# Optimization experiments

Measured on AMD Instinct MI355X. Metric: run time of the kernel, lower is better.

Reference implementation:

```python
import jax, jax.numpy as jnp
import numpy as np

EPS = 1e-3  # keras LayerNormalization default epsilon

def _layernorm(x, g, b):
    mu = jnp.mean(x, axis=-1, keepdims=True)
    var = jnp.mean(jnp.square(x - mu), axis=-1, keepdims=True)
    return (x - mu) * jax.lax.rsqrt(var + EPS) * g + b

def setup_inputs() -> dict:
    key = jax.random.key(0)
    ks = jax.random.split(key, 12)
    B, T, C = 2, 2048, 768
    s = 0.02
    return {
        "x": jax.random.normal(ks[0], (B, T, C), jnp.float32),
        "ln1_g": jnp.ones((C,), jnp.float32), "ln1_b": jnp.zeros((C,), jnp.float32),
        "Wq": jax.random.normal(ks[1], (C, C), jnp.float32) * s, "bq": jnp.zeros((C,), jnp.float32),
        "Wk": jax.random.normal(ks[2], (C, C), jnp.float32) * s, "bk": jnp.zeros((C,), jnp.float32),
        "Wv": jax.random.normal(ks[3], (C, C), jnp.float32) * s, "bv": jnp.zeros((C,), jnp.float32),
        "ln2_g": jnp.ones((C,), jnp.float32), "ln2_b": jnp.zeros((C,), jnp.float32),
        "W1": jax.random.normal(ks[4], (C, 4 * C), jnp.float32) * s, "b1": jnp.zeros((4 * C,), jnp.float32),
        "W2": jax.random.normal(ks[5], (4 * C, C), jnp.float32) * s, "b2": jnp.zeros((C,), jnp.float32),
    }

def reference(x, ln1_g, ln1_b, Wq, bq, Wk, bk, Wv, bv, ln2_g, ln2_b, W1, b1, W2, b2):
    H = 12
    B, T, C = x.shape
    dh = C // H
    # pre-LN (note: original overwrites x with LN output before residual)
    x = _layernorm(x, ln1_g, ln1_b)
    q = (x @ Wq + bq).reshape(B, T, H, dh).transpose(0, 2, 1, 3)
    k = (x @ Wk + bk).reshape(B, T, H, dh).transpose(0, 2, 1, 3)
    v = (x @ Wv + bv).reshape(B, T, H, dh).transpose(0, 2, 1, 3)
    # original computes K @ Q^T (transpose_b on query)
    scores = jnp.einsum('bhid,bhjd->bhij', k, q) / jnp.sqrt(jnp.float32(dh))
    mask = jnp.tril(jnp.ones((T, T), bool))
    scores = jnp.where(mask, scores, -jnp.inf)
    p = jax.nn.softmax(scores, axis=-1)
    y = jnp.einsum('bhij,bhjd->bhid', p, v)  # [B,H,T,dh]
    y = y.transpose(0, 2, 1, 3).reshape(B, T, C)
    x = x + y
    h = _layernorm(x, ln2_g, ln2_b)
    h = jax.nn.gelu(h @ W1 + b1, approximate=False)
    h = h @ W2 + b2
    return x + h
```

## Files before the change

kernel.cpp:

```cpp
#include <hip/hip_runtime.h>
#include <hip/hip_bf16.h>
#include <cmath>


#define BB 2
#define TT 2048
#define CC 768
#define HH 12
#define DH 64
#define NROWS (BB*TT)
#define NHEADS (BB*HH)

typedef __attribute__((ext_vector_type(8))) short bf16x8;
typedef __attribute__((ext_vector_type(4))) float f32x4;
typedef __attribute__((ext_vector_type(4))) unsigned short u16x4;

__device__ __forceinline__ unsigned short f2bf(float f){
  union { __hip_bfloat16 h; unsigned short u; } c;
  c.h = __float2bfloat16(f);
  return c.u;
}
__device__ __forceinline__ float bf2f(unsigned short u){
  union { unsigned int i; float f; } x; x.i = ((unsigned int)u) << 16; return x.f;
}
template<int BK>
__device__ __forceinline__ int swzk(int r, int c){
  if constexpr (BK == 64) return (r << 6) + (c ^ ((r & 7) << 3));
  else                    return (r << 5) + (c ^ (((r >> 1) & 3) << 3));
}
template<int BK>
__device__ __forceinline__ int swzsrc(int r, int c){
  if constexpr (BK == 64) return c ^ ((r & 7) << 3);
  else                    return c ^ (((r >> 1) & 3) << 3);
}
__device__ __forceinline__ float wred_sum(float v){
  #pragma unroll
  for(int m = 1; m < 64; m <<= 1) v += __shfl_xor(v, m, 64);
  return v;
}
__device__ __forceinline__ float gelu_fast(float x){
  float x2 = x * x;
  float e = x * fmaf(x2, 0.044715f, 1.0f) * 2.30203136f;
  float t = exp2f(e);
  return x - x / (t + 1.0f);
}
__device__ __forceinline__ void gload_lds16(const void* g, void* l){
  __builtin_amdgcn_global_load_lds((const __attribute__((address_space(1))) void*)g,
                                   (__attribute__((address_space(3))) void*)l, 16, 0, 0);
}
template<int N> __device__ __forceinline__ void waitcnt_vm(){
  if constexpr (N == 0)      asm volatile("s_waitcnt vmcnt(0)" ::: "memory");
  else if constexpr (N == 4) asm volatile("s_waitcnt vmcnt(4)" ::: "memory");
  else if constexpr (N == 8) asm volatile("s_waitcnt vmcnt(8)" ::: "memory");
  else static_assert(N == 0 || N == 4 || N == 8, "unsupported vmcnt");
}

#define SCLOG2 (0.125f * 1.44269504f)

__device__ __forceinline__ void tc_body(const float* __restrict__ in,
                                        unsigned short* __restrict__ out,
                                        int K, int N, int bx, int by,
                                        float (*tile)[33]){
  int n0 = bx * 32, k0 = by * 32;
  int t = threadIdx.x; int c = t & 31; int r0 = t >> 5;
  #pragma unroll
  for(int p = 0; p < 4; p++){
    int r = r0 + p * 8;
    tile[r][c] = in[(size_t)(k0 + r) * N + n0 + c];
  }
  __syncthreads();
  #pragma unroll
  for(int p = 0; p < 4; p++){
    int r = r0 + p * 8;
    out[(size_t)(n0 + r) * K + k0 + c] = f2bf(tile[c][r]);
  }
}

__device__ __forceinline__ void ln_body(const float* __restrict__ in,
                                        const float* __restrict__ gm,
                                        const float* __restrict__ bt,
                                        unsigned short* __restrict__ out_b,
                                        int r){
  int t = threadIdx.x;
  const float* row = in + (size_t)r * CC;
  float v0 = row[t], v1 = row[t + 256], v2 = row[t + 512];
  float s = wred_sum(v0 + v1 + v2);
  __shared__ float red[4];
  if((t & 63) == 0) red[t >> 6] = s;
  __syncthreads();
  float mu = (red[0] + red[1] + red[2] + red[3]) * (1.0f / CC);
  float d0 = v0 - mu, d1 = v1 - mu, d2 = v2 - mu;
  float q = wred_sum(d0 * d0 + d1 * d1 + d2 * d2);
  __shared__ float red2[4];
  if((t & 63) == 0) red2[t >> 6] = q;
  __syncthreads();
  float var = (red2[0] + red2[1] + red2[2] + red2[3]) * (1.0f / CC);
  float rinv = rsqrtf(var + 1e-3f);
  float o0 = d0 * rinv * gm[t]       + bt[t];
  float o1 = d1 * rinv * gm[t + 256] + bt[t + 256];
  float o2 = d2 * rinv * gm[t + 512] + bt[t + 512];
  size_t base = (size_t)r * CC;
  out_b[base + t] = f2bf(o0); out_b[base + t + 256] = f2bf(o1); out_b[base + t + 512] = f2bf(o2);
}

__global__ __launch_bounds__(256) void prep_ln_kernel(const float* __restrict__ Wq,
                                                      const float* __restrict__ Wk,
                                                      const float* __restrict__ Wv,
                                                      const float* __restrict__ W1,
                                                      const float* __restrict__ W2,
                                                      const float* __restrict__ bq,
                                                      const float* __restrict__ bk,
                                                      const float* __restrict__ bv,
                                                      const float* __restrict__ x,
                                                      const float* __restrict__ ln1g,
                                                      const float* __restrict__ ln1b,
                                                      unsigned short* __restrict__ wqkv,
                                                      unsigned short* __restrict__ w1t,
                                                      unsigned short* __restrict__ w2t,
                                                      float* __restrict__ bqkv,
                                                      unsigned short* __restrict__ xlnb){
  __shared__ float tile[32][33];
  int o = blockIdx.x;
  if(o < 1728){
    int z = o / 576, r = o % 576;
    const float* in = (z == 0) ? Wq : (z == 1) ? Wk : Wv;
    tc_body(in, wqkv + (size_t)z * CC * CC, CC, CC, r % 24, r / 24, tile);
  } else if(o < 4032){
    int r = o - 1728;
    tc_body(W1, w1t, CC, 4 * CC, r % 96, r / 96, tile);
  } else if(o < 6336){
    int r = o - 4032;
    tc_body(W2, w2t, 4 * CC, CC, r % 24, r / 24, tile);
  } else if(o < 6345){
    int i = (o - 6336) * 256 + threadIdx.x;
    if(i < 3 * CC) bqkv[i] = (i < CC) ? bq[i] : (i < 2 * CC) ? bk[i - CC] : bv[i - 2 * CC];
  } else {
    ln_body(x, ln1g, ln1b, xlnb, o - 6345);
  }
}

template<int MODE, int TILE, int BK>
__global__ __launch_bounds__(256) void gemm_bt(const unsigned short* __restrict__ A,
                                               const unsigned short* __restrict__ Bt,
                                               const float* __restrict__ bias,
                                               const float* __restrict__ resid,
                                               void* __restrict__ outp,
                                               unsigned short* __restrict__ vt,
                                               int M, int N, int K){
  constexpr int F = TILE / 32;
  constexpr int SEGS = TILE * BK / 512;
  constexpr int R = SEGS / 4;
  constexpr int NLD = 2 * R;
  constexpr int LPR = BK / 8;
  constexpr int RPS = 512 / BK;
  __shared__ unsigned short As[3][TILE * BK];
  __shared__ unsigned short Bs[3][TILE * BK];
  int m0 = blockIdx.y * TILE, n0 = blockIdx.x * TILE;
  int t = threadIdx.x; int w = t >> 6; int l = t & 63;
  int g = l >> 4; int lc = l & 15;
  int wm = w >> 1, wn = w & 1;
  f32x4 zero4 = {0.f, 0.f, 0.f, 0.f};
  f32x4 acc[F][F];
  #pragma unroll
  for(int mi = 0; mi < F; mi++)
    #pragma unroll
    for(int ni = 0; ni < F; ni++) acc[mi][ni] = zero4;

  auto stage = [&](int ks, int cb){
    #pragma unroll
    for(int p = 0; p < R; p++){
      int sgi = w * R + p;
      int r = sgi * RPS + l / LPR;
      int c = (l % LPR) * 8;
      int csrc = swzsrc<BK>(r, c);
      gload_lds16(A  + (size_t)(m0 + r) * K + ks + csrc, &As[cb][sgi * 512]);
      gload_lds16(Bt + (size_t)(n0 + r) * K + ks + csrc, &Bs[cb][sgi * 512]);
    }
  };

  int nt = K / BK;
  stage(0, 0);
  if(nt > 1) stage(BK, 1);
  if(nt > 2) stage(2 * BK, 2);
  int cur = 0;
  for(int ti = 0; ti < nt; ti++){
    if(ti + 2 < nt)      waitcnt_vm<2 * NLD>();
    else if(ti + 1 < nt) waitcnt_vm<NLD>();
    else                 waitcnt_vm<0>();
    __builtin_amdgcn_s_barrier();
    #pragma unroll
    for(int kk = 0; kk < BK / 32; kk++){
      bf16x8 af[F], bfv[F];
      #pragma unroll
      for(int mi = 0; mi < F; mi++) af[mi]  = *(const bf16x8*)&As[cur][swzk<BK>(wm * (TILE / 2) + mi * 16 + lc, kk * 32 + g * 8)];
      #pragma unroll
      for(int ni = 0; ni < F; ni++) bfv[ni] = *(const bf16x8*)&Bs[cur][swzk<BK>(wn * (TILE / 2) + ni * 16 + lc, kk * 32 + g * 8)];
      #pragma unroll
      for(int mi = 0; mi < F; mi++)
        #pragma unroll
        for(int ni = 0; ni < F; ni++)
          acc[mi][ni] = __builtin_amdgcn_mfma_f32_16x16x32_bf16(af[mi], bfv[ni], acc[mi][ni], 0, 0, 0);
    }
    __builtin_amdgcn_s_barrier();
    if(ti + 3 < nt) stage((ti + 3) * BK, cur);
    cur = (cur == 2) ? 0 : cur + 1;
  }
  #pragma unroll
  for(int mi = 0; mi < F; mi++)
    #pragma unroll
    for(int ni = 0; ni < F; ni++){
      int col = n0 + wn * (TILE / 2) + ni * 16 + lc;
      float bvv = bias[col];
      if(MODE == 3 && col >= 2 * CC){
        int hh = (col - 2 * CC) >> 6, d = (col - 2 * CC) & 63;
        int rowb = m0 + wm * (TILE / 2) + mi * 16 + g * 4;
        int bb = rowb >> 11, tb = rowb & 2047;
        u16x4 pk;
        #pragma unroll
        for(int rr = 0; rr < 4; rr++) pk[rr] = f2bf(acc[mi][ni][rr] + bvv);
        *(u16x4*)&vt[(((size_t)bb * HH + hh) * DH + d) * TT + tb] = pk;
      } else {
        #pragma unroll
        for(int rr = 0; rr < 4; rr++){
          int row = m0 + wm * (TILE / 2) + mi * 16 + g * 4 + rr;
          float v = acc[mi][ni][rr] + bvv;
          size_t idx = (size_t)row * N + col;
          if(MODE == 1) v = gelu_fast(v);
          if(MODE == 2) ((float*)outp)[idx] = v + resid[idx];
          else          ((unsigned short*)outp)[idx] = f2bf(v);
        }
      }
    }
}

__global__ __launch_bounds__(256) void attn_kernel(const unsigned short* __restrict__ qkv,
                                                   const unsigned short* __restrict__ vt,
                                                   unsigned short* __restrict__ po,
                                                   float* __restrict__ pl,
                                                   float* __restrict__ pm){
  __shared__ unsigned short Aq[2][64 * 64];
  __shared__ unsigned short Vs[2][64 * 64];
  __shared__ unsigned short Ps[4][16 * 64];
  int o = blockIdx.x;
  int xcd = o & 7, qq = o >> 3;
  int head = xcd * 3 + (qq % 3);
  int r_ = qq / 3;
  int bx = 31 - (r_ >> 1);
  int sp = r_ & 1;
  int b = head / HH, h = head % HH;
  int t = threadIdx.x; int w = t >> 6; int l = t & 63;
  int g = l >> 4, lc = l & 15;
  int i0w = bx * 64 + w * 16;
  int irow = i0w + lc;
  unsigned short* pw = &Ps[w][0];

  int hh = (bx + 2) >> 1;
  int js0 = sp ? hh : 0;
  int js1 = sp ? (bx + 1) : hh;

  int rl = l >> 3;
  int csrc = ((l & 7) * 8) ^ (rl * 8);

  bf16x8 bk[2];
  #pragma unroll
  for(int kk = 0; kk < 2; kk++)
    bk[kk] = *(const bf16x8*)(qkv + (size_t)(b * TT + irow) * (3 * CC) + CC + h * DH + kk * 32 + g * 8);

  float m_ = 0.0f, lsum = 0.f;
  f32x4 zero4 = {0.f, 0.f, 0.f, 0.f};
  f32x4 o4[4];
  #pragma unroll
  for(int ds = 0; ds < 4; ds++) o4[ds] = zero4;

  auto stage = [&](int j0, int cb){
    #pragma unroll
    for(int p = 0; p < 2; p++){
      int sgi = w * 2 + p;
      int row = sgi * 8 + rl;
      gload_lds16(qkv + (size_t)(b * TT + j0 + row) * (3 * CC) + h * DH + csrc, &Aq[cb][sgi * 512]);
      gload_lds16(vt  + (size_t)(head * DH + row) * TT + j0 + csrc,             &Vs[cb][sgi * 512]);
    }
  };

  if(js0 < js1){
    stage(js0 * 64, js0 & 1);
    if(js0 + 1 < js1) stage((js0 + 1) * 64, (js0 + 1) & 1);

    for(int jt = js0; jt < js1; jt++){
      int j0 = jt * 64;
      int buf = jt & 1;
      if(jt + 1 < js1) waitcnt_vm<4>(); else waitcnt_vm<0>();
      __builtin_amdgcn_s_barrier();
      f32x4 s[4];
      __builtin_amdgcn_s_setprio(1);
      #pragma unroll
      for(int js = 0; js < 4; js++){
        s[js] = zero4;
        #pragma unroll
        for(int kk = 0; kk < 2; kk++){
          bf16x8 aq = *(const bf16x8*)&Aq[buf][swzk<64>(js * 16 + lc, kk * 32 + g * 8)];
          s[js] = __builtin_amdgcn_mfma_f32_16x16x32_bf16(aq, bk[kk], s[js], 0, 0, 0);
        }
      }
      __builtin_amdgcn_s_setprio(0);
      if(j0 + 63 > i0w){
        #pragma unroll
        for(int js = 0; js < 4; js++)
          #pragma unroll
          for(int rr = 0; rr < 4; rr++){
            int j = j0 + js * 16 + g * 4 + rr;
            if(j > irow) s[js][rr] = -1e30f;
          }
      }
      float nmSC = -m_ * SCLOG2;
      f32x4 p[4];
      float rsum = 0.f;
      #pragma unroll
      for(int js = 0; js < 4; js++)
        #pragma unroll
        for(int rr = 0; rr < 4; rr++){
          float pv = exp2f(fmaf(s[js][rr], SCLOG2, nmSC));
          p[js][rr] = pv;
          rsum += pv;
        }
      rsum += __shfl_xor(rsum, 16, 64);
      rsum += __shfl_xor(rsum, 32, 64);
      if(__builtin_expect(__any(!(rsum < 1e30f)), 0)){
        float mx = -1e30f;
        #pragma unroll
        for(int js = 0; js < 4; js++)
          #pragma unroll
          for(int rr = 0; rr < 4; rr++) mx = fmaxf(mx, s[js][rr]);
        mx = fmaxf(mx, __shfl_xor(mx, 16, 64));
        mx = fmaxf(mx, __shfl_xor(mx, 32, 64));
        float mn = fmaxf(m_, mx);
        float al = exp2f((m_ - mn) * SCLOG2);
        m_ = mn;
        lsum *= al;
        #pragma unroll
        for(int rr = 0; rr < 4; rr++){
          float alb = __shfl(al, g * 4 + rr, 64);
          #pragma unroll
          for(int ds = 0; ds < 4; ds++) o4[ds][rr] *= alb;
        }
        nmSC = -m_ * SCLOG2;
        rsum = 0.f;
        #pragma unroll
        for(int js = 0; js < 4; js++)
          #pragma unroll
          for(int rr = 0; rr < 4; rr++){
            float pv = exp2f(fmaf(s[js][rr], SCLOG2, nmSC));
            p[js][rr] = pv;
            rsum += pv;
          }
        rsum += __shfl_xor(rsum, 16, 64);
        rsum += __shfl_xor(rsum, 32, 64);
      }
      lsum += rsum;
      #pragma unroll
      for(int js = 0; js < 4; js++){
        u16x4 pk;
        #pragma unroll
        for(int rr = 0; rr < 4; rr++) pk[rr] = f2bf(p[js][rr]);
        *(u16x4*)&pw[swzk<64>(lc, js * 16 + g * 4)] = pk;
      }
      bf16x8 pa[2];
      #pragma unroll
      for(int kk = 0; kk < 2; kk++)
        pa[kk] = *(const bf16x8*)&pw[swzk<64>(lc, kk * 32 + g * 8)];
      __builtin_amdgcn_s_setprio(1);
      #pragma unroll
      for(int ds = 0; ds < 4; ds++)
        #pragma unroll
        for(int kk = 0; kk < 2; kk++){
          bf16x8 vb = *(const bf16x8*)&Vs[buf][swzk<64>(ds * 16 + lc, kk * 32 + g * 8)];
          o4[ds] = __builtin_amdgcn_mfma_f32_16x16x32_bf16(pa[kk], vb, o4[ds], 0, 0, 0);
        }
      __builtin_amdgcn_s_setprio(0);
      __builtin_amdgcn_s_barrier();
      if(jt + 2 < js1) stage((jt + 2) * 64, buf);
    }
  }
  size_t pobase = (size_t)sp * (NHEADS * TT * DH) + (size_t)head * TT * DH;
  #pragma unroll
  for(int rr = 0; rr < 4; rr++){
    int ig = i0w + g * 4 + rr;
    #pragma unroll
    for(int ds = 0; ds < 4; ds++)
      po[pobase + (size_t)ig * DH + ds * 16 + lc] = f2bf(o4[ds][rr]);
  }
  if(g == 0){
    size_t pidx = (size_t)sp * (NHEADS * TT) + (size_t)head * TT + i0w + lc;
    pl[pidx] = lsum;
    pm[pidx] = m_;
  }
}

__global__ __launch_bounds__(256) void combine_ln2(const unsigned short* __restrict__ po,
                                                   const float* __restrict__ pl,
                                                   const float* __restrict__ pm,
                                                   const unsigned short* __restrict__ xlnb,
                                                   const float* __restrict__ gm,
                                                   const float* __restrict__ bt,
                                                   float* __restrict__ x1,
                                                   unsigned short* __restrict__ hln2){
  int r = blockIdx.x; int t = threadIdx.x;
  int b = r >> 11, i = r & 2047;
  float v[3];
  #pragma unroll
  for(int p = 0; p < 3; p++){
    int c = t + p * 256;
    int h = c >> 6, d = c & 63;
    size_t pidx = ((size_t)(b * HH + h)) * TT + i;
    float m0v = pm[pidx], m1v = pm[pidx + NHEADS * TT];
    float l0 = pl[pidx],  l1 = pl[pidx + NHEADS * TT];
    float M = fmaxf(m0v, m1v);
    float w0 = exp2f((m0v - M) * SCLOG2), w1 = exp2f((m1v - M) * SCLOG2);
    float p0 = bf2f(po[pidx * DH + d]);
    float p1 = bf2f(po[(size_t)NHEADS * TT * DH + pidx * DH + d]);
    float att = (p0 * w0 + p1 * w1) / (l0 * w0 + l1 * w1);
    v[p] = bf2f(xlnb[(size_t)r * CC + c]) + att;
  }
  float s = wred_sum(v[0] + v[1] + v[2]);
  __shared__ float red[4];
  if((t & 63) == 0) red[t >> 6] = s;
  __syncthreads();
  float mu = (red[0] + red[1] + red[2] + red[3]) * (1.0f / CC);
  float d0 = v[0] - mu, d1 = v[1] - mu, d2 = v[2] - mu;
  float q = wred_sum(d0 * d0 + d1 * d1 + d2 * d2);
  __shared__ float red2[4];
  if((t & 63) == 0) red2[t >> 6] = q;
  __syncthreads();
  float var = (red2[0] + red2[1] + red2[2] + red2[3]) * (1.0f / CC);
  float rinv = rsqrtf(var + 1e-3f);
  size_t base = (size_t)r * CC;
  x1[base + t] = v[0]; x1[base + t + 256] = v[1]; x1[base + t + 512] = v[2];
  hln2[base + t]       = f2bf(d0 * rinv * gm[t]       + bt[t]);
  hln2[base + t + 256] = f2bf(d1 * rinv * gm[t + 256] + bt[t + 256]);
  hln2[base + t + 512] = f2bf(d2 * rinv * gm[t + 512] + bt[t + 512]);
}

extern "C" void kernel_launch(void* const* d_in, const int* in_sizes, int n_in,
                              void* d_out, int out_size, void* d_ws, size_t ws_size,
                              hipStream_t stream){
  const float* x    = (const float*)d_in[0];
  const float* ln1g = (const float*)d_in[1];
  const float* ln1b = (const float*)d_in[2];
  const float* Wq   = (const float*)d_in[3];
  const float* bq   = (const float*)d_in[4];
  const float* Wk   = (const float*)d_in[5];
  const float* bk   = (const float*)d_in[6];
  const float* Wv   = (const float*)d_in[7];
  const float* bv   = (const float*)d_in[8];
  const float* ln2g = (const float*)d_in[9];
  const float* ln2b = (const float*)d_in[10];
  const float* W1   = (const float*)d_in[11];
  const float* b1   = (const float*)d_in[12];
  const float* W2   = (const float*)d_in[13];
  const float* b2   = (const float*)d_in[14];

  char* ws = (char*)d_ws;
  unsigned short* po   = (unsigned short*)(ws + 0);
  unsigned short* xlnb = (unsigned short*)(ws + 12582912);
  float*          x1   = (float*)(ws + 18874368);
  unsigned short* hln2 = (unsigned short*)(ws + 31457280);
  unsigned short* wqkv = (unsigned short*)(ws + 37748736);
  float*          bqkv = (float*)(ws + 41287680);
  unsigned short* w1t  = (unsigned short*)(ws + 41296896);
  unsigned short* w2t  = (unsigned short*)(ws + 46015488);
  unsigned short* qkv  = (unsigned short*)(ws + 50734080);
  unsigned short* vt   = (unsigned short*)(ws + 69608448);
  float*          pl   = (float*)(ws + 75899904);
  float*          pm   = (float*)(ws + 76293120);
  unsigned short* mlp1 = (unsigned short*)(ws + 50734080);

  prep_ln_kernel<<<dim3(6345 + NROWS), 256, 0, stream>>>(Wq, Wk, Wv, W1, W2, bq, bk, bv,
                                                         x, ln1g, ln1b,
                                                         wqkv, w1t, w2t, bqkv, xlnb);

  gemm_bt<3, 128, 32><<<dim3(18, 32), 256, 0, stream>>>(xlnb, wqkv, bqkv, nullptr, qkv, vt, NROWS, 3 * CC, CC);

  attn_kernel<<<dim3(1536), 256, 0, stream>>>(qkv, vt, po, pl, pm);

  combine_ln2<<<dim3(NROWS), 256, 0, stream>>>(po, pl, pm, xlnb, ln2g, ln2b, x1, hln2);

  gemm_bt<1, 128, 32><<<dim3(24, 32), 256, 0, stream>>>(hln2, w1t, b1, nullptr, mlp1, nullptr, NROWS, 4 * CC, CC);

  gemm_bt<2, 64, 64><<<dim3(12, 64), 256, 0, stream>>>(mlp1, w2t, b2, x1, d_out, nullptr, NROWS, CC, 4 * CC);

  (void)in_sizes; (void)n_in; (void)out_size; (void)ws_size;
}
```

Measured before the change: 159.0 us.

## Add dedicated 256x256-tile 512-thread GEMM kernel for MLP1 with fused GELU

Replaces the generic 128-tile GEMM used for the first MLP projection with a new kernel that uses 256x256 block tiles, 8 waves and 8x4 MFMA fragments per wave. Each wave does more MFMA work per LDS load, so LDS and global traffic per output element drop. The trade-off is a grid of only 192 blocks, which underfills a 256-CU MI355X, plus high register pressure from 32 accumulator vectors. The GELU that MODE 1 of the generic kernel applied is removed there, since that mode is no longer launched.

New measurement: 163.2 us. 1.03x slower.

```diff
diff --git a/kernel.cpp b/kernel.cpp
--- a/kernel.cpp
+++ b/kernel.cpp
@@ -225,10 +225,73 @@
           int row = m0 + wm * (TILE / 2) + mi * 16 + g * 4 + rr;
           float v = acc[mi][ni][rr] + bvv;
           size_t idx = (size_t)row * N + col;
-          if(MODE == 1) v = gelu_fast(v);
           if(MODE == 2) ((float*)outp)[idx] = v + resid[idx];
           else          ((unsigned short*)outp)[idx] = f2bf(v);
         }
+      }
+    }
+}
+
+__global__ __launch_bounds__(512, 2) void gemm256_gelu(const unsigned short* __restrict__ A,
+                                                       const unsigned short* __restrict__ Bt,
+                                                       const float* __restrict__ bias,
+                                                       unsigned short* __restrict__ outp,
+                                                       int M, int N, int K){
+  __shared__ unsigned short As[2][256 * 32];
+  __shared__ unsigned short Bs[2][256 * 32];
+  int m0 = blockIdx.y * 256, n0 = blockIdx.x * 256;
+  int t = threadIdx.x; int w = t >> 6; int l = t & 63;
+  int g = l >> 4; int lc = l & 15;
+  int wm = w >> 2, wn = w & 3;
+  f32x4 zero4 = {0.f, 0.f, 0.f, 0.f};
+  f32x4 acc[8][4];
+  #pragma unroll
+  for(int mi = 0; mi < 8; mi++)
+    #pragma unroll
+    for(int ni = 0; ni < 4; ni++) acc[mi][ni] = zero4;
+
+  auto stage = [&](int ks, int cb){
+    #pragma unroll
+    for(int p = 0; p < 2; p++){
+      int sgi = w * 2 + p;
+      int r = sgi * 16 + (l >> 2);
+      int c = (l & 3) * 8;
+      int csrc = swzsrc<32>(r, c);
+      gload_lds16(A  + (size_t)(m0 + r) * K + ks + csrc, &As[cb][sgi * 512]);
+      gload_lds16(Bt + (size_t)(n0 + r) * K + ks + csrc, &Bs[cb][sgi * 512]);
+    }
+  };
+
+  int nt = K >> 5;
+  stage(0, 0);
+  if(nt > 1) stage(32, 1);
+  for(int ti = 0; ti < nt; ti++){
+    if(ti + 1 < nt) waitcnt_vm<4>(); else waitcnt_vm<0>();
+    __builtin_amdgcn_s_barrier();
+    int cur = ti & 1;
+    bf16x8 af[8], bfv[4];
+    #pragma unroll
+    for(int mi = 0; mi < 8; mi++) af[mi]  = *(const bf16x8*)&As[cur][swzk<32>(wm * 128 + mi * 16 + lc, g * 8)];
+    #pragma unroll
+    for(int ni = 0; ni < 4; ni++) bfv[ni] = *(const bf16x8*)&Bs[cur][swzk<32>(wn * 64 + ni * 16 + lc, g * 8)];
+    #pragma unroll
+    for(int mi = 0; mi < 8; mi++)
+      #pragma unroll
+      for(int ni = 0; ni < 4; ni++)
+        acc[mi][ni] = __builtin_amdgcn_mfma_f32_16x16x32_bf16(af[mi], bfv[ni], acc[mi][ni], 0, 0, 0);
+    __builtin_amdgcn_s_barrier();
+    if(ti + 2 < nt) stage((ti + 2) * 32, cur);
+  }
+  #pragma unroll
+  for(int mi = 0; mi < 8; mi++)
+    #pragma unroll
+    for(int ni = 0; ni < 4; ni++){
+      int col = n0 + wn * 64 + ni * 16 + lc;
+      float bvv = bias[col];
+      #pragma unroll
+      for(int rr = 0; rr < 4; rr++){
+        int row = m0 + wm * 128 + mi * 16 + g * 4 + rr;
+        outp[(size_t)row * N + col] = f2bf(gelu_fast(acc[mi][ni][rr] + bvv));
       }
     }
 }
@@ -484,7 +547,7 @@
 
   combine_ln2<<<dim3(NROWS), 256, 0, stream>>>(po, pl, pm, xlnb, ln2g, ln2b, x1, hln2);
 
-  gemm_bt<1, 128, 32><<<dim3(24, 32), 256, 0, stream>>>(hln2, w1t, b1, nullptr, mlp1, nullptr, NROWS, 4 * CC, CC);
+  gemm256_gelu<<<dim3(12, 16), 512, 0, stream>>>(hln2, w1t, b1, mlp1, NROWS, 4 * CC, CC);
 
   gemm_bt<2, 64, 64><<<dim3(12, 64), 256, 0, stream>>>(mlp1, w2t, b2, x1, d_out, nullptr, NROWS, CC, 4 * CC);
 
```
